# Kernel optimization log

Measured on AMD Instinct MI355X. Metric: run time of the kernel, lower is better.

## Reference

```python
import jax, jax.numpy as jnp
import numpy as np

NUM_HEADS = 16
MASK_VALUE = -10000.0


def setup_inputs() -> dict:
    key = jax.random.key(0)
    ks = jax.random.split(key, 5)
    B, S, D = 2, 2048, 1024
    std = 0.02
    return {
        "hidden_states": jax.random.normal(ks[0], (B, S, D), dtype=jnp.float32),
        "wq": jax.random.normal(ks[1], (D, D), dtype=jnp.float32) * std,
        "bq": jnp.zeros((D,), dtype=jnp.float32),
        "wk": jax.random.normal(ks[2], (D, D), dtype=jnp.float32) * std,
        "bk": jnp.zeros((D,), dtype=jnp.float32),
        "wv": jax.random.normal(ks[3], (D, D), dtype=jnp.float32) * std,
        "bv": jnp.zeros((D,), dtype=jnp.float32),
        "wc": jax.random.normal(ks[4], (D, D), dtype=jnp.float32) * std,
        "bc": jnp.zeros((D,), dtype=jnp.float32),
    }


def reference(hidden_states, wq, bq, wk, bk, wv, bv, wc, bc):
    B, S, D = hidden_states.shape
    H = NUM_HEADS
    hd = D // H

    def split_heads(x):  # [B,S,D] -> [B,H,S,hd]
        return x.reshape(B, S, H, hd).transpose(0, 2, 1, 3)

    q = split_heads(hidden_states @ wq + bq)
    k = split_heads(hidden_states @ wk + bk)
    v = split_heads(hidden_states @ wv + bv)

    # eager QK^T with scale_attn_weights (divide by sqrt(head_dim))
    attn_weights = jnp.einsum("bhqd,bhkd->bhqk", q, k) / jnp.sqrt(
        jnp.asarray(hd, dtype=q.dtype))

    # causal mask (attention_mask is None, not cross-attention)
    causal = jnp.tril(jnp.ones((S, S), dtype=bool))[None, None]
    attn_weights = jnp.where(causal, attn_weights,
                             jnp.asarray(MASK_VALUE, dtype=attn_weights.dtype))

    attn_weights = jax.nn.softmax(attn_weights, axis=-1)
    # attn_dropout p=0.0 (eval) -> identity; no head_mask

    attn_output = jnp.einsum("bhqk,bhkd->bhqd", attn_weights, v)
    attn_output = attn_output.transpose(0, 2, 1, 3).reshape(B, S, D)
    attn_output = attn_output @ wc + bc  # c_proj; resid_dropout p=0 -> identity
    return attn_output, attn_weights, k, v
```

## Files before the change

### kernel.cpp

```cpp
#include <hip/hip_runtime.h>


typedef __attribute__((ext_vector_type(8))) short bf8_t;
typedef __attribute__((ext_vector_type(4))) float f4_t;
typedef __attribute__((ext_vector_type(8))) _Float16 h8_t;
typedef __attribute__((ext_vector_type(4))) _Float16 h4_t;

#define MFMA(a, b, c)  __builtin_amdgcn_mfma_f32_16x16x32_bf16(a, b, c, 0, 0, 0)
#define MFMAH(a, b, c) __builtin_amdgcn_mfma_f32_16x16x32_f16(a, b, c, 0, 0, 0)

static __device__ __forceinline__ unsigned short f2bf(float f) {
    union { float f; unsigned u; } x; x.f = f;
    unsigned u = x.u;
    return (unsigned short)((u + 0x7fffu + ((u >> 16) & 1u)) >> 16);
}

static __device__ __forceinline__ void stage16(const unsigned short* g, unsigned short* lbase) {
    __builtin_amdgcn_global_load_lds(
        (const __attribute__((address_space(1))) unsigned int*)g,
        (__attribute__((address_space(3))) unsigned int*)lbase, 16, 0, 0);
}

#define NE 4194304ULL
#define AW 134217728ULL


__global__ void cast_hidden(const float* __restrict__ src, unsigned short* __restrict__ dst) {
    int i = (blockIdx.x * 256 + threadIdx.x) * 4;
    float4 h = *(const float4*)(src + i);
    ushort4 o;
    o.x = f2bf(h.x); o.y = f2bf(h.y); o.z = f2bf(h.z); o.w = f2bf(h.w);
    *(ushort4*)(dst + i) = o;
}

__global__ void transpose_w(const float* __restrict__ wq, const float* __restrict__ wk,
                            const float* __restrict__ wv, const float* __restrict__ wc,
                            unsigned short* __restrict__ wqkvT, unsigned short* __restrict__ wcT) {
    __shared__ float tile[32][33];
    int z = blockIdx.z;
    const float* W = z == 0 ? wq : z == 1 ? wk : z == 2 ? wv : wc;
    unsigned short* dst = (z < 3) ? (wqkvT + (size_t)z * 1024 * 1024) : wcT;
    int x0 = blockIdx.x * 32, y0 = blockIdx.y * 32;
    int tx = threadIdx.x, ty = threadIdx.y;
#pragma unroll
    for (int i = 0; i < 4; ++i)
        tile[ty + i * 8][tx] = W[(size_t)(y0 + ty + i * 8) * 1024 + x0 + tx];
    __syncthreads();
#pragma unroll
    for (int i = 0; i < 4; ++i)
        dst[(size_t)(x0 + ty + i * 8) * 1024 + y0 + tx] = f2bf(tile[tx][ty + i * 8]);
}


#define GEMM_CORE(A_, B_, KDIM)                                                             \
    const int m0 = blockIdx.y * 128, n0 = blockIdx.x * 128;                                 \
    const int tid = threadIdx.x, w = tid >> 6, lane = tid & 63, ln = lane & 15,             \
              quad = lane >> 4;                                                             \
    const int wm = (w & 1) * 64, wn = (w >> 1) * 64;                                        \
    f4_t acc[4][4] = {};                                                                    \
    for (int kb = 0; kb < (KDIM); kb += 64) {                                               \
        __syncthreads();                                                                    \
        _Pragma("unroll")                                                                   \
        for (int p = 0; p < 4; ++p) {                                                       \
            int t = (w * 4 + p) * 64 + lane;                                                \
            int r = t >> 3, c = (t & 7) ^ (r & 7);                                          \
            stage16(&(A_)[(size_t)(m0 + r) * (KDIM) + kb + c * 8], &As[(w * 4 + p) * 512]); \
            stage16(&(B_)[(size_t)(n0 + r) * (KDIM) + kb + c * 8], &Bs[(w * 4 + p) * 512]); \
        }                                                                                   \
        __syncthreads();                                                                    \
        bf8_t af[2][4], bfm[2][4];                                                          \
        _Pragma("unroll")                                                                   \
        for (int h = 0; h < 2; ++h) {                                                       \
            _Pragma("unroll")                                                               \
            for (int i = 0; i < 4; ++i) {                                                   \
                int c = (h * 4 + quad) ^ (ln & 7);                                          \
                af[h][i] = *(const bf8_t*)&As[(wm + i * 16 + ln) * 64 + c * 8];             \
                bfm[h][i] = *(const bf8_t*)&Bs[(wn + i * 16 + ln) * 64 + c * 8];            \
            }                                                                               \
        }                                                                                   \
        _Pragma("unroll")                                                                   \
        for (int h = 0; h < 2; ++h)                                                         \
            _Pragma("unroll")                                                               \
            for (int i = 0; i < 4; ++i)                                                     \
                _Pragma("unroll")                                                           \
                for (int j = 0; j < 4; ++j)                                                 \
                    acc[i][j] = MFMA(af[h][i], bfm[h][j], acc[i][j]);                       \
    }

__global__ __launch_bounds__(256) void gemm_qkv(
    const unsigned short* __restrict__ A, const unsigned short* __restrict__ BT,
    const float* __restrict__ bq, const float* __restrict__ bk, const float* __restrict__ bv,
    unsigned short* __restrict__ q_bf, unsigned short* __restrict__ k_bf,
    _Float16* __restrict__ vT_h, float* __restrict__ out_k, float* __restrict__ out_v)
{
    __shared__ __align__(16) unsigned short As[128 * 64];
    __shared__ __align__(16) unsigned short Bs[128 * 64];
    GEMM_CORE(A, BT, 1024)
#pragma unroll
    for (int j = 0; j < 4; ++j) {
        int coln = n0 + wn + j * 16 + ln;
        int which = coln >> 10, d = coln & 1023, h = d >> 6, e = d & 63;
        float bias = which == 0 ? bq[d] : (which == 1 ? bk[d] : bv[d]);
#pragma unroll
        for (int i = 0; i < 4; ++i) {
#pragma unroll
            for (int v = 0; v < 4; ++v) {
                int row = m0 + wm + i * 16 + quad * 4 + v;
                int b = row >> 11, s = row & 2047;
                float val = acc[i][j][v] + bias;
                size_t hidx = (((size_t)(b * 16 + h)) * 2048 + s) * 64 + e;
                if (which == 0) {
                    q_bf[hidx] = f2bf(val * 0.125f);
                } else if (which == 1) {
                    k_bf[hidx] = f2bf(val);
                    __builtin_nontemporal_store(val, &out_k[hidx]);
                } else {
                    vT_h[((size_t)(b * 16 + h) * 64 + e) * 2048 + s] = (_Float16)val;
                    __builtin_nontemporal_store(val, &out_v[hidx]);
                }
            }
        }
    }
}

__global__ __launch_bounds__(256) void gemm_cproj(
    const unsigned short* __restrict__ A, const unsigned short* __restrict__ BT,
    const float* __restrict__ bc, float* __restrict__ out)
{
    __shared__ __align__(16) unsigned short As[128 * 64];
    __shared__ __align__(16) unsigned short Bs[128 * 64];
    GEMM_CORE(A, BT, 1024)
#pragma unroll
    for (int j = 0; j < 4; ++j) {
        int coln = n0 + wn + j * 16 + ln;
        float bias = bc[coln];
#pragma unroll
        for (int i = 0; i < 4; ++i) {
#pragma unroll
            for (int v = 0; v < 4; ++v) {
                int row = m0 + wm + i * 16 + quad * 4 + v;
                __builtin_nontemporal_store(acc[i][j][v] + bias, &out[(size_t)row * 1024 + coln]);
            }
        }
    }
}

#define PB 2068

__global__ __launch_bounds__(512) void attn_fused(
    const unsigned short* __restrict__ q_bf,
    const unsigned short* __restrict__ k_bf,
    const _Float16* __restrict__ vT_h,
    float* __restrict__ attn_w,
    unsigned short* __restrict__ attnpre)
{
    __shared__ _Float16 Pbuf[16 * PB];
    __shared__ float oatom[16][68];
    __shared__ float lred[16];
    const int bh = blockIdx.x;
    const int g0 = (127 - (int)blockIdx.y) * 16;
    const int tid = threadIdx.x, w = tid >> 6, lane = tid & 63, ln = lane & 15, quad = lane >> 4;

    if (tid < 16) lred[tid] = 0.f;
#pragma unroll
    for (int i = 0; i < 3; ++i) {
        int s = tid + i * 512;
        if (s < 16 * 68) ((float*)oatom)[s] = 0.f;
    }
    __syncthreads();

    const unsigned short* qb = q_bf + ((size_t)bh * 2048 + g0) * 64;
    bf8_t aA0 = *(const bf8_t*)&qb[(size_t)ln * 64 + quad * 8];
    bf8_t aA1 = *(const bf8_t*)&qb[(size_t)ln * 64 + 32 + quad * 8];
    const unsigned short* kb_base = k_bf + (size_t)bh * 2048 * 64;
    const _Float16* vt_base = vT_h + (size_t)bh * 64 * 2048;
    const f4_t zf = {0.f, 0.f, 0.f, 0.f};
    const int cend = ((g0 + 16 + 31) >> 5) << 5;
    const int b = bh >> 4, h = bh & 15;

    f4_t lv = {0.f, 0.f, 0.f, 0.f};
    f4_t o[4] = {};
    for (int c = w * 32; c < cend; c += 256) {
        bf8_t kf[4];
        h8_t vb[4];
#pragma unroll
        for (int sub = 0; sub < 2; ++sub) {
            const unsigned short* kp = kb_base + (size_t)(c + sub * 16 + ln) * 64 + quad * 8;
            kf[sub * 2] = *(const bf8_t*)kp;
            kf[sub * 2 + 1] = *(const bf8_t*)(kp + 32);
        }
#pragma unroll
        for (int j = 0; j < 4; ++j)
            vb[j] = *(const h8_t*)(vt_base + (size_t)(j * 16 + ln) * 2048 + c + quad * 8);
#pragma unroll
        for (int sub = 0; sub < 2; ++sub) {
            f4_t sc = MFMA(aA0, kf[sub * 2], zf);
            sc = MFMA(aA1, kf[sub * 2 + 1], sc);
            int col = c + sub * 16 + ln;
#pragma unroll
            for (int v = 0; v < 4; ++v) {
                int row = g0 + quad * 4 + v;
                float p = (col <= row) ? __expf(sc[v]) : 0.f;
                lv[v] += p;
                Pbuf[(quad * 4 + v) * PB + col] = (_Float16)p;
            }
        }
        h8_t pf = *(const h8_t*)&Pbuf[ln * PB + c + quad * 8];
#pragma unroll
        for (int j = 0; j < 4; ++j) o[j] = MFMAH(pf, vb[j], o[j]);
    }

#pragma unroll
    for (int m = 1; m < 16; m <<= 1) {
#pragma unroll
        for (int v = 0; v < 4; ++v) lv[v] += __shfl_xor(lv[v], m);
    }
    if (ln == 0) {
#pragma unroll
        for (int v = 0; v < 4; ++v) atomicAdd(&lred[quad * 4 + v], lv[v]);
    }
#pragma unroll
    for (int j = 0; j < 4; ++j)
#pragma unroll
        for (int v = 0; v < 4; ++v)
            atomicAdd(&oatom[quad * 4 + v][j * 16 + ln], o[j][v]);
    __syncthreads();

    float* awp = attn_w + ((size_t)bh * 2048 + g0) * 2048;
#pragma unroll
    for (int rr = 0; rr < 2; ++rr) {
        int row = w * 2 + rr;
        float linv_r = 1.f / lred[row];
        float* dst = awp + (size_t)row * 2048;
#pragma unroll
        for (int i = 0; i < 8; ++i) {
            int col = i * 256 + lane * 4;
            h4_t ph = *(const h4_t*)&Pbuf[row * PB + col];
            f4_t val;
#pragma unroll
            for (int j = 0; j < 4; ++j)
                val[j] = (col + j < cend) ? (float)ph[j] * linv_r : 0.f;
            __builtin_nontemporal_store(val, (f4_t*)(dst + col));
        }
    }

#pragma unroll
    for (int rr = 0; rr < 2; ++rr) {
        int row = w * 2 + rr;
        float linv_r = 1.f / lred[row];
        attnpre[(size_t)(b * 2048 + g0 + row) * 1024 + h * 64 + lane] =
            f2bf(oatom[row][lane] * linv_r);
    }
}

extern "C" void kernel_launch(void* const* d_in, const int* in_sizes, int n_in,
                              void* d_out, int out_size, void* d_ws, size_t ws_size,
                              hipStream_t stream)
{
    const float* hs = (const float*)d_in[0];
    const float* wq = (const float*)d_in[1];
    const float* bq = (const float*)d_in[2];
    const float* wk = (const float*)d_in[3];
    const float* bk = (const float*)d_in[4];
    const float* wv = (const float*)d_in[5];
    const float* bv = (const float*)d_in[6];
    const float* wc = (const float*)d_in[7];
    const float* bc = (const float*)d_in[8];

    float* out      = (float*)d_out;
    float* out_aw   = out + NE;
    float* out_k    = out_aw + AW;
    float* out_v    = out_k + NE;

    char* ws = (char*)d_ws;
    unsigned short* hid_bf  = (unsigned short*)(ws);
    unsigned short* wqkvT   = (unsigned short*)(ws + 8388608);
    unsigned short* wcT     = (unsigned short*)(ws + 14680064);
    unsigned short* q_bf    = (unsigned short*)(ws + 16777216);
    unsigned short* k_bf    = (unsigned short*)(ws + 25165824);
    _Float16*       vT_h    = (_Float16*)(ws + 33554432);
    unsigned short* attnpre = (unsigned short*)(ws + 41943040);

    cast_hidden<<<4096, 256, 0, stream>>>(hs, hid_bf);
    transpose_w<<<dim3(32, 32, 4), dim3(32, 8), 0, stream>>>(wq, wk, wv, wc, wqkvT, wcT);
    gemm_qkv<<<dim3(24, 32), 256, 0, stream>>>(hid_bf, wqkvT, bq, bk, bv,
                                               q_bf, k_bf, vT_h, out_k, out_v);
    attn_fused<<<dim3(32, 128), 512, 0, stream>>>(q_bf, k_bf, vT_h, out_aw, attnpre);
    gemm_cproj<<<dim3(8, 32), 256, 0, stream>>>(attnpre, wcT, bc, out);
}
```

Before: 827.8 us.

## Shrink attention query tile to 8 rows with fp32 probability buffer

The fused attention kernel now handles 8 query rows per block instead of 16, doubling the grid and reordering it so query tiles vary fastest. The shared-memory probability buffer holds fp32 values instead of fp16, which keeps attention weights at full precision and halves the rows stored. Zero padding is written to shared memory so the output loop can store rows with straight vector copies. This brings more blocks and less shared memory per block, but half the MFMA rows are wasted and the K/V rereads per query row double.

New measurement: 1.082 ms. 1.31x slower.

```diff
diff --git a/kernel.cpp b/kernel.cpp
--- a/kernel.cpp
+++ b/kernel.cpp
@@ -4,7 +4,6 @@
 typedef __attribute__((ext_vector_type(8))) short bf8_t;
 typedef __attribute__((ext_vector_type(4))) float f4_t;
 typedef __attribute__((ext_vector_type(8))) _Float16 h8_t;
-typedef __attribute__((ext_vector_type(4))) _Float16 h4_t;
 
 #define MFMA(a, b, c)  __builtin_amdgcn_mfma_f32_16x16x32_bf16(a, b, c, 0, 0, 0)
 #define MFMAH(a, b, c) __builtin_amdgcn_mfma_f32_16x16x32_f16(a, b, c, 0, 0, 0)
@@ -145,7 +144,7 @@
     }
 }
 
-#define PB 2068
+#define PS 2052
 
 __global__ __launch_bounds__(512) void attn_fused(
     const unsigned short* __restrict__ q_bf,
@@ -154,11 +153,11 @@
     float* __restrict__ attn_w,
     unsigned short* __restrict__ attnpre)
 {
-    __shared__ _Float16 Pbuf[16 * PB];
+    __shared__ __align__(16) float Pbuf[8 * PS];
     __shared__ float oatom[16][68];
     __shared__ float lred[16];
-    const int bh = blockIdx.x;
-    const int g0 = (127 - (int)blockIdx.y) * 16;
+    const int bh = blockIdx.y;
+    const int g0 = (255 - (int)blockIdx.x) * 8;
     const int tid = threadIdx.x, w = tid >> 6, lane = tid & 63, ln = lane & 15, quad = lane >> 4;
 
     if (tid < 16) lred[tid] = 0.f;
@@ -170,12 +169,12 @@
     __syncthreads();
 
     const unsigned short* qb = q_bf + ((size_t)bh * 2048 + g0) * 64;
-    bf8_t aA0 = *(const bf8_t*)&qb[(size_t)ln * 64 + quad * 8];
-    bf8_t aA1 = *(const bf8_t*)&qb[(size_t)ln * 64 + 32 + quad * 8];
+    bf8_t aA0 = *(const bf8_t*)&qb[(size_t)(ln & 7) * 64 + quad * 8];
+    bf8_t aA1 = *(const bf8_t*)&qb[(size_t)(ln & 7) * 64 + 32 + quad * 8];
     const unsigned short* kb_base = k_bf + (size_t)bh * 2048 * 64;
     const _Float16* vt_base = vT_h + (size_t)bh * 64 * 2048;
     const f4_t zf = {0.f, 0.f, 0.f, 0.f};
-    const int cend = ((g0 + 16 + 31) >> 5) << 5;
+    const int cend = ((g0 + 8 + 31) >> 5) << 5;
     const int b = bh >> 4, h = bh & 15;
 
     f4_t lv = {0.f, 0.f, 0.f, 0.f};
@@ -202,12 +201,23 @@
                 int row = g0 + quad * 4 + v;
                 float p = (col <= row) ? __expf(sc[v]) : 0.f;
                 lv[v] += p;
-                Pbuf[(quad * 4 + v) * PB + col] = (_Float16)p;
+                if (quad < 2) Pbuf[(quad * 4 + v) * PS + col] = p;
             }
         }
-        h8_t pf = *(const h8_t*)&Pbuf[ln * PB + c + quad * 8];
+        f4_t pa = *(const f4_t*)&Pbuf[(ln & 7) * PS + c + quad * 8];
+        f4_t pb = *(const f4_t*)&Pbuf[(ln & 7) * PS + c + quad * 8 + 4];
+        h8_t pf;
+        pf[0] = (_Float16)pa[0]; pf[1] = (_Float16)pa[1];
+        pf[2] = (_Float16)pa[2]; pf[3] = (_Float16)pa[3];
+        pf[4] = (_Float16)pb[0]; pf[5] = (_Float16)pb[1];
+        pf[6] = (_Float16)pb[2]; pf[7] = (_Float16)pb[3];
 #pragma unroll
         for (int j = 0; j < 4; ++j) o[j] = MFMAH(pf, vb[j], o[j]);
+    }
+
+    const int pzend = (cend + 255) & ~255;
+    {
+        for (int c = cend + lane; c < pzend; c += 64) Pbuf[w * PS + c] = 0.f;
     }
 
 #pragma unroll
@@ -226,31 +236,25 @@
             atomicAdd(&oatom[quad * 4 + v][j * 16 + ln], o[j][v]);
     __syncthreads();
 
-    float* awp = attn_w + ((size_t)bh * 2048 + g0) * 2048;
-#pragma unroll
-    for (int rr = 0; rr < 2; ++rr) {
-        int row = w * 2 + rr;
-        float linv_r = 1.f / lred[row];
-        float* dst = awp + (size_t)row * 2048;
-#pragma unroll
-        for (int i = 0; i < 8; ++i) {
-            int col = i * 256 + lane * 4;
-            h4_t ph = *(const h4_t*)&Pbuf[row * PB + col];
-            f4_t val;
-#pragma unroll
-            for (int j = 0; j < 4; ++j)
-                val[j] = (col + j < cend) ? (float)ph[j] * linv_r : 0.f;
+    const int row = w;
+    const float linv_r = 1.f / lred[row];
+    float* dst = attn_w + ((size_t)bh * 2048 + g0 + row) * 2048;
+    const int nread = pzend >> 8;
+    const float* psrc = &Pbuf[row * PS];
+#pragma unroll
+    for (int i = 0; i < 8; ++i) {
+        int col = i * 256 + lane * 4;
+        if (i < nread) {
+            f4_t val = *(const f4_t*)&psrc[col];
+            val[0] *= linv_r; val[1] *= linv_r; val[2] *= linv_r; val[3] *= linv_r;
             __builtin_nontemporal_store(val, (f4_t*)(dst + col));
-        }
-    }
-
-#pragma unroll
-    for (int rr = 0; rr < 2; ++rr) {
-        int row = w * 2 + rr;
-        float linv_r = 1.f / lred[row];
-        attnpre[(size_t)(b * 2048 + g0 + row) * 1024 + h * 64 + lane] =
-            f2bf(oatom[row][lane] * linv_r);
-    }
+        } else {
+            __builtin_nontemporal_store(zf, (f4_t*)(dst + col));
+        }
+    }
+
+    attnpre[(size_t)(b * 2048 + g0 + row) * 1024 + h * 64 + lane] =
+        f2bf(oatom[row][lane] * linv_r);
 }
 
 extern "C" void kernel_launch(void* const* d_in, const int* in_sizes, int n_in,
@@ -285,6 +289,6 @@
     transpose_w<<<dim3(32, 32, 4), dim3(32, 8), 0, stream>>>(wq, wk, wv, wc, wqkvT, wcT);
     gemm_qkv<<<dim3(24, 32), 256, 0, stream>>>(hid_bf, wqkvT, bq, bk, bv,
                                                q_bf, k_bf, vT_h, out_k, out_v);
-    attn_fused<<<dim3(32, 128), 512, 0, stream>>>(q_bf, k_bf, vT_h, out_aw, attnpre);
+    attn_fused<<<dim3(256, 32), 512, 0, stream>>>(q_bf, k_bf, vT_h, out_aw, attnpre);
     gemm_cproj<<<dim3(8, 32), 256, 0, stream>>>(attnpre, wcT, bc, out);
 }
```
